# Performance work log

Measured on AMD Instinct MI355X. Metric: run time of the kernel, lower is better.

## Reference

```python
import jax, jax.numpy as jnp
import numpy as np

P0, P1, P2 = 0, 9, 95          # player, status
P3 = 103                        # player_info end / cards start
P4 = P3 + 13 * 740              # 9723, cards end / potions start
P5 = P4 + 43                    # 9766, relics start
P6 = P5 + 180                   # 9946, monsters start
P7 = P6 + 5 * 101               # 10451


def setup_inputs() -> dict:
    key = jax.random.key(0)
    ks = jax.random.split(key, 8)
    def lin(k, out_f, in_f):
        # torch.nn.Linear default init: U(-1/sqrt(in), 1/sqrt(in)), weight [out, in]
        bound = 1.0 / np.sqrt(in_f)
        return jax.random.uniform(k, (out_f, in_f), jnp.float32, -bound, bound)
    return {
        "battle": jax.random.normal(ks[0], (32768, P7), jnp.float32),
        "W_player": lin(ks[1], 4, 9),
        "W_status": lin(ks[2], 16, 86),
        "W_pinfo": lin(ks[3], 2, 8),
        "W_card": lin(ks[4], 32, 740),
        "W_potions": lin(ks[5], 8, 43),
        "W_relics": lin(ks[6], 16, 180),
        "W_monster": lin(ks[7], 16, 101),
    }


def reference(battle, W_player, W_status, W_pinfo, W_card, W_potions, W_relics, W_monster):
    B = battle.shape[0]
    player = battle[:, P0:P1] @ W_player.T                     # [B, 4]
    status = battle[:, P1:P2] @ W_status.T                     # [B, 16]
    pinfo = battle[:, P2:P3] @ W_pinfo.T                       # [B, 2]
    # 13 card segments share one weight -> single batched GEMM
    cards = battle[:, P3:P4].reshape(B, 13, 740)
    cards = jnp.einsum('bsf,of->bso', cards, W_card).reshape(B, 13 * 32)
    potions = battle[:, P4:P5] @ W_potions.T                   # [B, 8]
    relics = battle[:, P5:P6] @ W_relics.T                     # [B, 16]
    # 5 monster segments share one weight
    monsters = battle[:, P6:P7].reshape(B, 5, 101)
    monsters = jnp.einsum('bsf,of->bso', monsters, W_monster).reshape(B, 5 * 16)
    # concat in the module's ModuleList order
    return jnp.concatenate([player, status, pinfo, cards, potions, relics, monsters], axis=-1)
```

## Files before the change

### kernel.cpp

```cpp
#include <hip/hip_runtime.h>
#include <stdint.h>


typedef __attribute__((ext_vector_type(8))) short short8;
typedef __attribute__((ext_vector_type(4))) float f32x4;

__device__ inline unsigned short f2bf(float f) {
  union { float f; uint32_t u; } v; v.f = f;
  uint32_t r = v.u + 0x7FFFu + ((v.u >> 16) & 1u);
  return (unsigned short)(r >> 16);
}

__device__ inline uint32_t cvt2(float lo, float hi) {
  uint32_t r;
  asm("v_cvt_pk_bf16_f32 %0, %1, %2" : "=v"(r) : "v"(lo), "v"(hi));
  return r;
}

union bfrag { short8 s; uint32_t u[4]; };

__device__ inline short8 mk_frag(f32x4 lo, f32x4 hi) {
  bfrag f;
  f.u[0] = cvt2(lo[0], lo[1]);
  f.u[1] = cvt2(lo[2], lo[3]);
  f.u[2] = cvt2(hi[0], hi[1]);
  f.u[3] = cvt2(hi[2], hi[3]);
  return f.s;
}

__device__ inline void gload_dw(const float* g, float* lds) {
  __builtin_amdgcn_global_load_lds(
      (const __attribute__((address_space(1))) void*)g,
      (__attribute__((address_space(3))) void*)lds, 4, 0, 0);
}

__global__ __launch_bounds__(256) void pack_w(const float* __restrict__ Wc,
                                              uint32_t* __restrict__ wout) {
  int el = blockIdx.x * 256 + threadIdx.x;
  if (el >= 12288) return;
  int d  = el & 3;
  int rl = (el >> 2) & 15;
  int kg = (el >> 6) & 3;
  int wn = (el >> 8) & 1;
  int cs = el >> 9;
  int n  = wn * 16 + rl;
  int k  = cs * 32 + kg * 8 + d * 2;
  float v0 = (k     < 740) ? Wc[n * 740 + k]     : 0.0f;
  float v1 = (k + 1 < 740) ? Wc[n * 740 + k + 1] : 0.0f;
  wout[el] = (uint32_t)f2bf(v0) | ((uint32_t)f2bf(v1) << 16);
}

__global__ __launch_bounds__(256, 4) void seg_gemm(
    const float* __restrict__ battle,
    const float* __restrict__ Wplayer, const float* __restrict__ Wstatus,
    const float* __restrict__ Wpinfo,  const float* __restrict__ Wpotions,
    const float* __restrict__ Wrelics, const float* __restrict__ Wmonster,
    const uint32_t* __restrict__ wpack2,
    float* __restrict__ out, const float* __restrict__ zpage)
{
  __shared__ float shm[10240];
  const int bid  = blockIdx.x;
  const int t    = threadIdx.x;
  const int lane = t & 63;
  const int wv   = t >> 6;
  const int rl   = lane & 15;
  const int kg   = lane >> 4;

  if (bid < 32768) {
    const uint32_t g0 = (uint32_t)bid * 10451u + 103u;
    #pragma unroll
    for (int r = 0; r < 38; ++r)
      gload_dw(battle + g0 + (uint32_t)(r * 256 + t), &shm[r * 256 + t]);
    __syncthreads();

    const int wn = wv & 1;
    const int wk = wv >> 1;
    const uint32_t abase = (rl < 13) ? (uint32_t)(rl * 740) : 0u;
    float* wred = &shm[9728];

    f32x4 acc = {0.f, 0.f, 0.f, 0.f};
    #pragma unroll
    for (int si = 0; si < 12; ++si) {
      const int cs = wk * 12 + si;
      const float* ap = shm + abase + (uint32_t)(cs * 32 + kg * 8);
      f32x4 lo = *(const f32x4*)ap;
      f32x4 hi = *(const f32x4*)(ap + 4);
      short8 aa = mk_frag(lo, hi);
      short8 wf = *(const short8*)(wpack2 + (uint32_t)(cs * 512 + wn * 256 + kg * 64 + rl * 4));
      acc = __builtin_amdgcn_mfma_f32_16x16x32_bf16(aa, wf, acc, 0, 0, 0);
    }

    if (wk == 1) {
      #pragma unroll
      for (int q = 0; q < 4; ++q)
        wred[wn * 256 + (kg * 4 + q) * 16 + rl] = acc[q];
    }
    __syncthreads();
    if (wk == 0) {
      const uint32_t ob = (uint32_t)bid * 542u + 22u;
      #pragma unroll
      for (int q = 0; q < 4; ++q) {
        const int sub = kg * 4 + q;
        float v = acc[q] + wred[wn * 256 + (kg * 4 + q) * 16 + rl];
        if (sub < 13)
          out[ob + (uint32_t)(sub * 32 + wn * 16 + rl)] = v;
      }
    }
    return;
  }

  const int sb = bid - 32768;
  int bloc, nsub, K, NOUT, soff, ooff;
  const float* wp;
  if (sb < 1280)      { bloc = sb;        nsub = 5; K = 101; NOUT = 16; soff = 9946; ooff = 462; wp = Wmonster; }
  else if (sb < 1536) { bloc = sb - 1280; nsub = 1; K = 180; NOUT = 16; soff = 9766; ooff = 446; wp = Wrelics; }
  else if (sb < 1792) { bloc = sb - 1536; nsub = 1; K = 86;  NOUT = 16; soff = 9;    ooff = 4;   wp = Wstatus; }
  else if (sb < 2048) { bloc = sb - 1792; nsub = 1; K = 43;  NOUT = 8;  soff = 9723; ooff = 438; wp = Wpotions; }
  else if (sb < 2304) { bloc = sb - 2048; nsub = 1; K = 9;   NOUT = 4;  soff = 0;    ooff = 0;   wp = Wplayer; }
  else                { bloc = sb - 2304; nsub = 1; K = 8;   NOUT = 2;  soff = 95;   ooff = 20;  wp = Wpinfo; }

  float* lds_a = shm;
  float* lds_w = shm + 4096;

  const int mb = bloc * 128;
  const int r0 = t >> 5;

  uint32_t rb[16];
  #pragma unroll
  for (int i = 0; i < 16; ++i) {
    uint32_t m   = (uint32_t)(mb + r0 + 8 * i);
    uint32_t b   = m / (uint32_t)nsub;
    uint32_t sub = m - b * (uint32_t)nsub;
    rb[i] = b * 10451u + (uint32_t)soff + sub * (uint32_t)K;
  }

  const int klin = t & 31;
  const int lk   = (((klin >> 2) ^ r0) << 2) | (klin & 3);

  f32x4 acc[2] = {};
  const int nch = (K + 31) >> 5;

  for (int ch = 0; ch < nch; ++ch) {
    const int kk = (ch << 5) + lk;
    #pragma unroll
    for (int i = 0; i < 16; ++i) {
      const float* sp = (kk < K) ? (battle + rb[i] + kk) : zpage;
      gload_dw(sp, &lds_a[i * 256 + t]);
    }
    #pragma unroll
    for (int i = 0; i < 4; ++i) {
      const int col = r0 + 8 * i;
      const float* sp = (col < NOUT && kk < K) ? (wp + col * K + kk) : zpage;
      gload_dw(sp, &lds_w[i * 256 + t]);
    }
    __syncthreads();

    short8 af[2], bfr;
    #pragma unroll
    for (int mf = 0; mf < 2; ++mf) {
      const int rr  = wv * 32 + mf * 16 + rl;
      const int g0i = (2 * kg) ^ (rr & 7);
      const int g1i = (2 * kg + 1) ^ (rr & 7);
      f32x4 lo = *(const f32x4*)&lds_a[rr * 32 + g0i * 4];
      f32x4 hi = *(const f32x4*)&lds_a[rr * 32 + g1i * 4];
      af[mf] = mk_frag(lo, hi);
    }
    {
      const int c   = rl;
      const int g0i = (2 * kg) ^ (c & 7);
      const int g1i = (2 * kg + 1) ^ (c & 7);
      f32x4 lo = *(const f32x4*)&lds_w[c * 32 + g0i * 4];
      f32x4 hi = *(const f32x4*)&lds_w[c * 32 + g1i * 4];
      bfr = mk_frag(lo, hi);
    }
    #pragma unroll
    for (int mf = 0; mf < 2; ++mf)
      acc[mf] = __builtin_amdgcn_mfma_f32_16x16x32_bf16(af[mf], bfr, acc[mf], 0, 0, 0);

    __syncthreads();
  }

  #pragma unroll
  for (int mf = 0; mf < 2; ++mf) {
    #pragma unroll
    for (int q = 0; q < 4; ++q) {
      uint32_t m   = (uint32_t)(mb + wv * 32 + mf * 16 + kg * 4 + q);
      uint32_t b   = m / (uint32_t)nsub;
      uint32_t sub = m - b * (uint32_t)nsub;
      uint32_t ob  = b * 542u + (uint32_t)ooff + sub * (uint32_t)NOUT;
      const int col = rl;
      if (col < NOUT) out[ob + col] = acc[mf][q];
    }
  }
}

extern "C" void kernel_launch(void* const* d_in, const int* in_sizes, int n_in,
                              void* d_out, int out_size, void* d_ws, size_t ws_size,
                              hipStream_t stream) {
  const float* battle   = (const float*)d_in[0];
  const float* Wplayer  = (const float*)d_in[1];
  const float* Wstatus  = (const float*)d_in[2];
  const float* Wpinfo   = (const float*)d_in[3];
  const float* Wcard    = (const float*)d_in[4];
  const float* Wpotions = (const float*)d_in[5];
  const float* Wrelics  = (const float*)d_in[6];
  const float* Wmonster = (const float*)d_in[7];
  float* out = (float*)d_out;

  const float* zpage = (const float*)d_ws;
  uint32_t* wpack2 = (uint32_t*)((char*)d_ws + 256);

  hipMemsetAsync(d_ws, 0, 256, stream);
  hipLaunchKernelGGL(pack_w, dim3(48), dim3(256), 0, stream, Wcard, wpack2);
  hipLaunchKernelGGL(seg_gemm, dim3(35328), dim3(256), 0, stream,
                     battle, Wplayer, Wstatus, Wpinfo, Wpotions, Wrelics,
                     Wmonster, (const uint32_t*)wpack2, out, zpage);
}
```

Baseline: 301.8 us.

## Process eight card rows per block with register-staged double-buffered LDS loads

After: 305.6 us. Within noise of the previous version (+1.3%).

```diff
diff --git a/kernel.cpp b/kernel.cpp
--- a/kernel.cpp
+++ b/kernel.cpp
@@ -4,6 +4,7 @@
 
 typedef __attribute__((ext_vector_type(8))) short short8;
 typedef __attribute__((ext_vector_type(4))) float f32x4;
+typedef __attribute__((ext_vector_type(4), aligned(4))) float f32x4u;
 
 __device__ inline unsigned short f2bf(float f) {
   union { float f; uint32_t u; } v; v.f = f;
@@ -50,7 +51,7 @@
   wout[el] = (uint32_t)f2bf(v0) | ((uint32_t)f2bf(v1) << 16);
 }
 
-__global__ __launch_bounds__(256, 4) void seg_gemm(
+__global__ __launch_bounds__(256, 2) void seg_gemm(
     const float* __restrict__ battle,
     const float* __restrict__ Wplayer, const float* __restrict__ Wstatus,
     const float* __restrict__ Wpinfo,  const float* __restrict__ Wpotions,
@@ -58,7 +59,7 @@
     const uint32_t* __restrict__ wpack2,
     float* __restrict__ out, const float* __restrict__ zpage)
 {
-  __shared__ float shm[10240];
+  __shared__ float shm[19968];
   const int bid  = blockIdx.x;
   const int t    = threadIdx.x;
   const int lane = t & 63;
@@ -66,50 +67,85 @@
   const int rl   = lane & 15;
   const int kg   = lane >> 4;
 
-  if (bid < 32768) {
-    const uint32_t g0 = (uint32_t)bid * 10451u + 103u;
-    #pragma unroll
-    for (int r = 0; r < 38; ++r)
-      gload_dw(battle + g0 + (uint32_t)(r * 256 + t), &shm[r * 256 + t]);
-    __syncthreads();
-
+  if (bid < 4096) {
+    const int row0 = bid * 8;
     const int wn = wv & 1;
     const int wk = wv >> 1;
-    const uint32_t abase = (rl < 13) ? (uint32_t)(rl * 740) : 0u;
-    float* wred = &shm[9728];
-
-    f32x4 acc = {0.f, 0.f, 0.f, 0.f};
+    float* wred = &shm[19456];
+
+    short8 wfr[12];
     #pragma unroll
     for (int si = 0; si < 12; ++si) {
       const int cs = wk * 12 + si;
-      const float* ap = shm + abase + (uint32_t)(cs * 32 + kg * 8);
-      f32x4 lo = *(const f32x4*)ap;
-      f32x4 hi = *(const f32x4*)(ap + 4);
-      short8 aa = mk_frag(lo, hi);
-      short8 wf = *(const short8*)(wpack2 + (uint32_t)(cs * 512 + wn * 256 + kg * 64 + rl * 4));
-      acc = __builtin_amdgcn_mfma_f32_16x16x32_bf16(aa, wf, acc, 0, 0, 0);
-    }
-
-    if (wk == 1) {
+      wfr[si] = *(const short8*)(wpack2 + (uint32_t)(cs * 512 + wn * 256 + kg * 64 + rl * 4));
+    }
+
+    f32x4 sreg[10];
+    #define LOADR(r_) do {                                                      \
+      const uint32_t row_el_ = (uint32_t)(row0 + (r_)) * 10451u + 103u;         \
+      const uint32_t b4_ = row_el_ & ~3u;                                       \
+      _Pragma("unroll")                                                         \
+      for (int rr = 0; rr < 9; ++rr)                                            \
+        sreg[rr] = *(const f32x4u*)(battle + b4_ + (uint32_t)(rr * 1024 + t * 4)); \
+      if (t < 128)                                                              \
+        sreg[9] = *(const f32x4u*)(battle + b4_ + (uint32_t)(9216 + t * 4));    \
+    } while (0)
+    #define WRITEB(buf_) do {                                                   \
+      _Pragma("unroll")                                                         \
+      for (int rr = 0; rr < 9; ++rr)                                            \
+        *(f32x4*)&(buf_)[rr * 1024 + t * 4] = sreg[rr];                         \
+      if (t < 128)                                                              \
+        *(f32x4*)&(buf_)[9216 + t * 4] = sreg[9];                               \
+    } while (0)
+
+    LOADR(0);
+    WRITEB(&shm[0]);
+    __syncthreads();
+
+    for (int r = 0; r < 8; ++r) {
+      const int cur = r & 1;
+      if (r + 1 < 8) LOADR(r + 1);
+
+      const uint32_t row_el = (uint32_t)(row0 + r) * 10451u + 103u;
+      const uint32_t delta  = row_el & 3u;
+      const float* abuf = &shm[cur * 9728];
+      const uint32_t abase = delta + ((rl < 13) ? (uint32_t)(rl * 740) : 0u);
+
+      f32x4 acc = {0.f, 0.f, 0.f, 0.f};
       #pragma unroll
-      for (int q = 0; q < 4; ++q)
-        wred[wn * 256 + (kg * 4 + q) * 16 + rl] = acc[q];
-    }
-    __syncthreads();
-    if (wk == 0) {
-      const uint32_t ob = (uint32_t)bid * 542u + 22u;
-      #pragma unroll
-      for (int q = 0; q < 4; ++q) {
-        const int sub = kg * 4 + q;
-        float v = acc[q] + wred[wn * 256 + (kg * 4 + q) * 16 + rl];
-        if (sub < 13)
-          out[ob + (uint32_t)(sub * 32 + wn * 16 + rl)] = v;
+      for (int si = 0; si < 12; ++si) {
+        const int cs = wk * 12 + si;
+        const float* ap = abuf + abase + (uint32_t)(cs * 32 + kg * 8);
+        f32x4 lo = *(const f32x4u*)ap;
+        f32x4 hi = *(const f32x4u*)(ap + 4);
+        short8 aa = mk_frag(lo, hi);
+        acc = __builtin_amdgcn_mfma_f32_16x16x32_bf16(aa, wfr[si], acc, 0, 0, 0);
       }
+
+      if (wk == 1) {
+        #pragma unroll
+        for (int q = 0; q < 4; ++q)
+          wred[wn * 256 + (kg * 4 + q) * 16 + rl] = acc[q];
+      }
+      __syncthreads();
+      if (wk == 0) {
+        const uint32_t ob = (uint32_t)(row0 + r) * 542u + 22u;
+        #pragma unroll
+        for (int q = 0; q < 4; ++q) {
+          const int sub = kg * 4 + q;
+          float v = acc[q] + wred[wn * 256 + (kg * 4 + q) * 16 + rl];
+          if (sub < 13)
+            out[ob + (uint32_t)(sub * 32 + wn * 16 + rl)] = v;
+        }
+      }
+
+      if (r + 1 < 8) WRITEB(&shm[(cur ^ 1) * 9728]);
+      __syncthreads();
     }
     return;
   }
 
-  const int sb = bid - 32768;
+  const int sb = bid - 4096;
   int bloc, nsub, K, NOUT, soff, ooff;
   const float* wp;
   if (sb < 1280)      { bloc = sb;        nsub = 5; K = 101; NOUT = 16; soff = 9946; ooff = 462; wp = Wmonster; }
@@ -212,7 +248,7 @@
 
   hipMemsetAsync(d_ws, 0, 256, stream);
   hipLaunchKernelGGL(pack_w, dim3(48), dim3(256), 0, stream, Wcard, wpack2);
-  hipLaunchKernelGGL(seg_gemm, dim3(35328), dim3(256), 0, stream,
+  hipLaunchKernelGGL(seg_gemm, dim3(6656), dim3(256), 0, stream,
                      battle, Wplayer, Wstatus, Wpinfo, Wpotions, Wrelics,
                      Wmonster, (const uint32_t*)wpack2, out, zpage);
 }
```

## Fuse small-segment GEMMs into per-row card block with prepacked bf16 weights

Applied to the files above, without the earlier changes.

New measurement: 301.9 us. About the same (+0.1%).

```diff
diff --git a/kernel.cpp b/kernel.cpp
--- a/kernel.cpp
+++ b/kernel.cpp
@@ -34,164 +34,140 @@
       (__attribute__((address_space(3))) void*)lds, 4, 0, 0);
 }
 
-__global__ __launch_bounds__(256) void pack_w(const float* __restrict__ Wc,
-                                              uint32_t* __restrict__ wout) {
+__global__ __launch_bounds__(256) void pack_w(
+    const float* __restrict__ Wp, const float* __restrict__ Ws,
+    const float* __restrict__ Wpi, const float* __restrict__ Wc,
+    const float* __restrict__ Wpo, const float* __restrict__ Wr,
+    const float* __restrict__ Wm, uint32_t* __restrict__ wout) {
   int el = blockIdx.x * 256 + threadIdx.x;
-  if (el >= 12288) return;
+  if (el >= 20992) return;
   int d  = el & 3;
   int rl = (el >> 2) & 15;
   int kg = (el >> 6) & 3;
   int wn = (el >> 8) & 1;
-  int cs = el >> 9;
-  int n  = wn * 16 + rl;
-  int k  = cs * 32 + kg * 8 + d * 2;
-  float v0 = (k     < 740) ? Wc[n * 740 + k]     : 0.0f;
-  float v1 = (k + 1 < 740) ? Wc[n * 740 + k + 1] : 0.0f;
+  int chunk = el >> 9;
+  const float* w; int K, NOUT, cbase;
+  if (chunk < 24)      { w = Wc;  K = 740; NOUT = 32; cbase = 0; }
+  else if (chunk < 27) { w = Ws;  K = 86;  NOUT = 16; cbase = 24; }
+  else if (chunk < 29) { w = Wpo; K = 43;  NOUT = 8;  cbase = 27; }
+  else if (chunk < 30) { w = Wp;  K = 9;   NOUT = 4;  cbase = 29; }
+  else if (chunk < 31) { w = Wpi; K = 8;   NOUT = 2;  cbase = 30; }
+  else if (chunk < 35) { w = Wm;  K = 101; NOUT = 16; cbase = 31; }
+  else                 { w = Wr;  K = 180; NOUT = 16; cbase = 35; }
+  int n = wn * 16 + rl;
+  int k = (chunk - cbase) * 32 + kg * 8 + d * 2;
+  float v0 = (n < NOUT && k     < K) ? w[n * K + k]     : 0.0f;
+  float v1 = (n < NOUT && k + 1 < K) ? w[n * K + k + 1] : 0.0f;
   wout[el] = (uint32_t)f2bf(v0) | ((uint32_t)f2bf(v1) << 16);
 }
 
-__global__ __launch_bounds__(256, 4) void seg_gemm(
+__global__ __launch_bounds__(256, 3) void seg_gemm(
     const float* __restrict__ battle,
-    const float* __restrict__ Wplayer, const float* __restrict__ Wstatus,
-    const float* __restrict__ Wpinfo,  const float* __restrict__ Wpotions,
-    const float* __restrict__ Wrelics, const float* __restrict__ Wmonster,
     const uint32_t* __restrict__ wpack2,
-    float* __restrict__ out, const float* __restrict__ zpage)
+    float* __restrict__ out)
 {
-  __shared__ float shm[10240];
-  const int bid  = blockIdx.x;
+  __shared__ float shm[11120];
+  const int b    = blockIdx.x;
   const int t    = threadIdx.x;
   const int lane = t & 63;
   const int wv   = t >> 6;
   const int rl   = lane & 15;
   const int kg   = lane >> 4;
+  const int wn   = wv & 1;
+  const int wk   = wv >> 1;
 
-  if (bid < 32768) {
-    const uint32_t g0 = (uint32_t)bid * 10451u + 103u;
-    #pragma unroll
-    for (int r = 0; r < 38; ++r)
-      gload_dw(battle + g0 + (uint32_t)(r * 256 + t), &shm[r * 256 + t]);
-    __syncthreads();
+  const uint32_t row = (uint32_t)b * 10451u;
 
-    const int wn = wv & 1;
-    const int wk = wv >> 1;
-    const uint32_t abase = (rl < 13) ? (uint32_t)(rl * 740) : 0u;
-    float* wred = &shm[9728];
+  #pragma unroll
+  for (int r = 0; r < 38; ++r)
+    gload_dw(battle + row + 103u + (uint32_t)(r * 256 + t), &shm[r * 256 + t]);
 
-    f32x4 acc = {0.f, 0.f, 0.f, 0.f};
-    #pragma unroll
-    for (int si = 0; si < 12; ++si) {
-      const int cs = wk * 12 + si;
-      const float* ap = shm + abase + (uint32_t)(cs * 32 + kg * 8);
-      f32x4 lo = *(const f32x4*)ap;
-      f32x4 hi = *(const f32x4*)(ap + 4);
-      short8 aa = mk_frag(lo, hi);
-      short8 wf = *(const short8*)(wpack2 + (uint32_t)(cs * 512 + wn * 256 + kg * 64 + rl * 4));
-      acc = __builtin_amdgcn_mfma_f32_16x16x32_bf16(aa, wf, acc, 0, 0, 0);
+  #pragma unroll
+  for (int r = 0; r < 4; ++r) {
+    const int s = r * 256 + t;
+    if (s < 880) {
+      int src;
+      if (s < 12)        src = s;
+      else if (s < 100)  src = 9 + (s - 12);
+      else if (s < 112)  src = 95 + (s - 100);
+      else if (s < 156)  src = 9723 + (s - 112);
+      else if (s < 336)  src = 9766 + (s - 156);
+      else if (s < 856) {
+        int sub = (s - 336) / 104;
+        int kk  = (s - 336) - sub * 104;
+        src = 9946 + sub * 101 + ((kk > 100) ? 100 : kk);
+      } else src = 0;
+      gload_dw(battle + row + (uint32_t)src, &shm[9728 + s]);
     }
+  }
+  __syncthreads();
 
-    if (wk == 1) {
-      #pragma unroll
-      for (int q = 0; q < 4; ++q)
-        wred[wn * 256 + (kg * 4 + q) * 16 + rl] = acc[q];
-    }
-    __syncthreads();
-    if (wk == 0) {
-      const uint32_t ob = (uint32_t)bid * 542u + 22u;
-      #pragma unroll
-      for (int q = 0; q < 4; ++q) {
-        const int sub = kg * 4 + q;
-        float v = acc[q] + wred[wn * 256 + (kg * 4 + q) * 16 + rl];
-        if (sub < 13)
-          out[ob + (uint32_t)(sub * 32 + wn * 16 + rl)] = v;
-      }
-    }
-    return;
+  const uint32_t abase = (rl < 13) ? (uint32_t)(rl * 740) : 0u;
+  float* wred = &shm[10608];
+
+  f32x4 acc = {0.f, 0.f, 0.f, 0.f};
+  #pragma unroll
+  for (int si = 0; si < 12; ++si) {
+    const int cs = wk * 12 + si;
+    const float* ap = shm + abase + (uint32_t)(cs * 32 + kg * 8);
+    f32x4 lo = *(const f32x4*)ap;
+    f32x4 hi = *(const f32x4*)(ap + 4);
+    short8 aa = mk_frag(lo, hi);
+    short8 wf = *(const short8*)(wpack2 + (uint32_t)(cs * 512 + wn * 256 + kg * 64 + rl * 4));
+    acc = __builtin_amdgcn_mfma_f32_16x16x32_bf16(aa, wf, acc, 0, 0, 0);
   }
 
-  const int sb = bid - 32768;
-  int bloc, nsub, K, NOUT, soff, ooff;
-  const float* wp;
-  if (sb < 1280)      { bloc = sb;        nsub = 5; K = 101; NOUT = 16; soff = 9946; ooff = 462; wp = Wmonster; }
-  else if (sb < 1536) { bloc = sb - 1280; nsub = 1; K = 180; NOUT = 16; soff = 9766; ooff = 446; wp = Wrelics; }
-  else if (sb < 1792) { bloc = sb - 1536; nsub = 1; K = 86;  NOUT = 16; soff = 9;    ooff = 4;   wp = Wstatus; }
-  else if (sb < 2048) { bloc = sb - 1792; nsub = 1; K = 43;  NOUT = 8;  soff = 9723; ooff = 438; wp = Wpotions; }
-  else if (sb < 2304) { bloc = sb - 2048; nsub = 1; K = 9;   NOUT = 4;  soff = 0;    ooff = 0;   wp = Wplayer; }
-  else                { bloc = sb - 2304; nsub = 1; K = 8;   NOUT = 2;  soff = 95;   ooff = 20;  wp = Wpinfo; }
+  if (wk == 1) {
+    #pragma unroll
+    for (int q = 0; q < 4; ++q)
+      wred[wn * 256 + (kg * 4 + q) * 16 + rl] = acc[q];
+  }
+  __syncthreads();
 
-  float* lds_a = shm;
-  float* lds_w = shm + 4096;
-
-  const int mb = bloc * 128;
-  const int r0 = t >> 5;
-
-  uint32_t rb[16];
-  #pragma unroll
-  for (int i = 0; i < 16; ++i) {
-    uint32_t m   = (uint32_t)(mb + r0 + 8 * i);
-    uint32_t b   = m / (uint32_t)nsub;
-    uint32_t sub = m - b * (uint32_t)nsub;
-    rb[i] = b * 10451u + (uint32_t)soff + sub * (uint32_t)K;
+  const uint32_t ob0 = (uint32_t)b * 542u;
+  if (wk == 0) {
+    #pragma unroll
+    for (int q = 0; q < 4; ++q) {
+      const int sub = kg * 4 + q;
+      float v = acc[q] + wred[wn * 256 + (kg * 4 + q) * 16 + rl];
+      if (sub < 13)
+        out[ob0 + 22u + (uint32_t)(sub * 32 + wn * 16 + rl)] = v;
+    }
   }
 
-  const int klin = t & 31;
-  const int lk   = (((klin >> 2) ^ r0) << 2) | (klin & 3);
+  #define DO_SEG(CBASE, NCH, SBOFF, STRIDE, M, NOUTS, OOFF) do {               \
+    f32x4 sacc = {0.f, 0.f, 0.f, 0.f};                                         \
+    _Pragma("unroll")                                                          \
+    for (int c = 0; c < (NCH); ++c) {                                          \
+      const uint32_t ab = 9728u + (SBOFF) +                                    \
+                          ((rl < (M)) ? (uint32_t)(rl * (STRIDE)) : 0u);       \
+      const float* ap = shm + ab + (uint32_t)(c * 32 + kg * 8);                \
+      f32x4 lo = *(const f32x4*)ap;                                            \
+      f32x4 hi = *(const f32x4*)(ap + 4);                                      \
+      short8 aa = mk_frag(lo, hi);                                             \
+      short8 wf = *(const short8*)(wpack2 +                                    \
+                    (uint32_t)(((CBASE) + c) * 512 + kg * 64 + rl * 4));       \
+      sacc = __builtin_amdgcn_mfma_f32_16x16x32_bf16(aa, wf, sacc, 0, 0, 0);   \
+    }                                                                          \
+    _Pragma("unroll")                                                          \
+    for (int q = 0; q < 4; ++q) {                                              \
+      const int rowq = kg * 4 + q;                                             \
+      if (rowq < (M) && rl < (NOUTS))                                          \
+        out[ob0 + (OOFF) + (uint32_t)(rowq * (NOUTS) + rl)] = sacc[q];         \
+    }                                                                          \
+  } while (0)
 
-  f32x4 acc[2] = {};
-  const int nch = (K + 31) >> 5;
-
-  for (int ch = 0; ch < nch; ++ch) {
-    const int kk = (ch << 5) + lk;
-    #pragma unroll
-    for (int i = 0; i < 16; ++i) {
-      const float* sp = (kk < K) ? (battle + rb[i] + kk) : zpage;
-      gload_dw(sp, &lds_a[i * 256 + t]);
-    }
-    #pragma unroll
-    for (int i = 0; i < 4; ++i) {
-      const int col = r0 + 8 * i;
-      const float* sp = (col < NOUT && kk < K) ? (wp + col * K + kk) : zpage;
-      gload_dw(sp, &lds_w[i * 256 + t]);
-    }
-    __syncthreads();
-
-    short8 af[2], bfr;
-    #pragma unroll
-    for (int mf = 0; mf < 2; ++mf) {
-      const int rr  = wv * 32 + mf * 16 + rl;
-      const int g0i = (2 * kg) ^ (rr & 7);
-      const int g1i = (2 * kg + 1) ^ (rr & 7);
-      f32x4 lo = *(const f32x4*)&lds_a[rr * 32 + g0i * 4];
-      f32x4 hi = *(const f32x4*)&lds_a[rr * 32 + g1i * 4];
-      af[mf] = mk_frag(lo, hi);
-    }
-    {
-      const int c   = rl;
-      const int g0i = (2 * kg) ^ (c & 7);
-      const int g1i = (2 * kg + 1) ^ (c & 7);
-      f32x4 lo = *(const f32x4*)&lds_w[c * 32 + g0i * 4];
-      f32x4 hi = *(const f32x4*)&lds_w[c * 32 + g1i * 4];
-      bfr = mk_frag(lo, hi);
-    }
-    #pragma unroll
-    for (int mf = 0; mf < 2; ++mf)
-      acc[mf] = __builtin_amdgcn_mfma_f32_16x16x32_bf16(af[mf], bfr, acc[mf], 0, 0, 0);
-
-    __syncthreads();
+  if (wv == 0) {
+    DO_SEG(24, 3, 12u,  0, 1, 16, 4u);
+    DO_SEG(27, 2, 112u, 0, 1, 8,  438u);
+    DO_SEG(29, 1, 0u,   0, 1, 4,  0u);
+    DO_SEG(30, 1, 100u, 0, 1, 2,  20u);
+  } else if (wv == 1) {
+    DO_SEG(31, 4, 336u, 104, 5, 16, 462u);
+  } else if (wv == 2) {
+    DO_SEG(35, 6, 156u, 0, 1, 16, 446u);
   }
-
-  #pragma unroll
-  for (int mf = 0; mf < 2; ++mf) {
-    #pragma unroll
-    for (int q = 0; q < 4; ++q) {
-      uint32_t m   = (uint32_t)(mb + wv * 32 + mf * 16 + kg * 4 + q);
-      uint32_t b   = m / (uint32_t)nsub;
-      uint32_t sub = m - b * (uint32_t)nsub;
-      uint32_t ob  = b * 542u + (uint32_t)ooff + sub * (uint32_t)NOUT;
-      const int col = rl;
-      if (col < NOUT) out[ob + col] = acc[mf][q];
-    }
-  }
+  #undef DO_SEG
 }
 
 extern "C" void kernel_launch(void* const* d_in, const int* in_sizes, int n_in,
@@ -207,12 +183,11 @@
   const float* Wmonster = (const float*)d_in[7];
   float* out = (float*)d_out;
 
-  const float* zpage = (const float*)d_ws;
-  uint32_t* wpack2 = (uint32_t*)((char*)d_ws + 256);
+  uint32_t* wpack2 = (uint32_t*)d_ws;
 
-  hipMemsetAsync(d_ws, 0, 256, stream);
-  hipLaunchKernelGGL(pack_w, dim3(48), dim3(256), 0, stream, Wcard, wpack2);
-  hipLaunchKernelGGL(seg_gemm, dim3(35328), dim3(256), 0, stream,
-                     battle, Wplayer, Wstatus, Wpinfo, Wpotions, Wrelics,
-                     Wmonster, (const uint32_t*)wpack2, out, zpage);
+  hipLaunchKernelGGL(pack_w, dim3(82), dim3(256), 0, stream,
+                     Wplayer, Wstatus, Wpinfo, Wcard, Wpotions, Wrelics,
+                     Wmonster, wpack2);
+  hipLaunchKernelGGL(seg_gemm, dim3(32768), dim3(256), 0, stream,
+                     battle, (const uint32_t*)wpack2, out);
 }
```
